# Kernel tuning notes

Measured on AMD Instinct MI355X. Metric: run time of the kernel, lower is better.

The kernel has to match this reference:

```python
import jax, jax.numpy as jnp
import numpy as np

B, T, D = 32, 1024, 1024
H = 512        # LSTM units per direction
L = 3          # num_layers


def _run_lstm(x, mask, W, U, b):
    """Masked unidirectional LSTM, Keras gate order (i, f, c, o).
    x: [B,T,D], mask: [B,T] bool (True = valid). Masked steps carry state
    and repeat the previous output, matching Keras masking semantics."""
    z_all = jnp.einsum('btd,dk->tbk', x, W) + b          # [T,B,4H]
    m_all = jnp.transpose(mask, (1, 0))                   # [T,B]

    def step(carry, inp):
        h, c = carry
        z_t, m_t = inp
        z = z_t + h @ U                                   # [B,4H]
        i, f, g, o = jnp.split(z, 4, axis=-1)
        i = jax.nn.sigmoid(i)
        f = jax.nn.sigmoid(f)
        g = jnp.tanh(g)
        o = jax.nn.sigmoid(o)
        c_new = f * c + i * g
        h_new = o * jnp.tanh(c_new)
        m = m_t[:, None]
        h = jnp.where(m, h_new, h)
        c = jnp.where(m, c_new, c)
        return (h, c), h

    h0 = jnp.zeros((x.shape[0], U.shape[0]), x.dtype)
    (_, _), hs = jax.lax.scan(step, (h0, h0), (z_all, m_all))
    return jnp.transpose(hs, (1, 0, 2))                   # [B,T,H]


def _bilstm(x, mask, Wf, Uf, bf, Wb, Ub, bb):
    fwd = _run_lstm(x, mask, Wf, Uf, bf)
    bwd = _run_lstm(x[:, ::-1], mask[:, ::-1], Wb, Ub, bb)[:, ::-1]
    return jnp.concatenate([fwd, bwd], axis=-1)           # [B,T,2H]


def setup_inputs() -> dict:
    key = jax.random.key(0)
    ks = jax.random.split(key, 16)
    s = 0.05
    inp = {
        'x': jax.random.normal(ks[0], (B, T, D), jnp.float32),
        'x_mask': jax.random.randint(ks[1], (B, T), 0, 2, jnp.int32),
        # stacked BiLSTM params (all layers share shapes since 2H == D)
        'Wf': jax.random.normal(ks[2], (L, D, 4 * H), jnp.float32) * s,
        'Uf': jax.random.normal(ks[3], (L, H, 4 * H), jnp.float32) * s,
        'bf': jax.random.normal(ks[4], (L, 4 * H), jnp.float32) * s,
        'Wb': jax.random.normal(ks[5], (L, D, 4 * H), jnp.float32) * s,
        'Ub': jax.random.normal(ks[6], (L, H, 4 * H), jnp.float32) * s,
        'bb': jax.random.normal(ks[7], (L, 4 * H), jnp.float32) * s,
        # task heads
        'Wp': jax.random.normal(ks[8], (2 * H, 2), jnp.float32) * s,
        'bp': jnp.zeros((2,), jnp.float32),
        'Wbu': jax.random.normal(ks[9], (2 * H, 2), jnp.float32) * s,
        'bbu': jnp.zeros((2,), jnp.float32),
        'Wss3': jax.random.normal(ks[10], (2 * H, 3), jnp.float32) * s,
        'bss3': jnp.zeros((3,), jnp.float32),
        'Wss8': jax.random.normal(ks[11], (2 * H, 8), jnp.float32) * s,
        'bss8': jnp.zeros((8,), jnp.float32),
        'training': 0,
    }
    return inp


def reference(x, x_mask, Wf, Uf, bf, Wb, Ub, bb, Wp, bp, Wbu, bbu,
              Wss3, bss3, Wss8, bss8, training):
    # mask = not(x_mask == 1): True = valid position
    mask = x_mask != 1
    for l in range(L):
        x = _bilstm(x, mask, Wf[l], Uf[l], bf[l], Wb[l], Ub[l], bb[l])
    x = jax.nn.relu(x)
    # dropout is identity at inference (training == 0)
    ppi = jax.nn.softmax(x @ Wp + bp, axis=-1)
    buried = x @ Wbu + bbu
    ss3 = x @ Wss3 + bss3
    ss8 = x @ Wss8 + bss8
    return (ppi, buried, ss3, ss8)
```

## Files before the change

### kernel.cpp

```cpp
#include <hip/hip_runtime.h>
#include <hip/hip_bf16.h>
#include <math.h>


#define B_ 32
#define T_ 1024
#define H_ 512
#define NG 2048

typedef __attribute__((ext_vector_type(8))) short bf16x8;
typedef __attribute__((ext_vector_type(4))) float f32x4;
typedef unsigned int u32;
typedef unsigned long long u64;
typedef unsigned short u16;

__device__ inline u16 f2bf(float f) {
    u32 u = __float_as_uint(f);
    return (u16)((u + 0x7fffu + ((u >> 16) & 1u)) >> 16);
}
__device__ inline float bf2f(u16 v) { return __uint_as_float(((u32)v) << 16); }
__device__ inline void gload16(const void* g, void* l) {
    __builtin_amdgcn_global_load_lds(
        (const __attribute__((address_space(1))) u32*)g,
        (__attribute__((address_space(3))) u32*)l, 16, 0, 0);
}
__device__ inline float fsig(float x) { return 1.0f / (1.0f + __expf(-x)); }
__device__ inline float ftanh(float x) { return 1.0f - 2.0f / (__expf(2.0f * x) + 1.0f); }

__global__ void zero_mem(float* __restrict__ s, int n) {
    int i = blockIdx.x * 256 + threadIdx.x;
    if (i < n) s[i] = 0.0f;
}

__global__ __launch_bounds__(256) void conv_bf16(const float* __restrict__ src,
                                                 u16* __restrict__ dst) {
    int i = blockIdx.x * 256 + threadIdx.x;
    float4 v = *(const float4*)&src[(size_t)i * 4];
    ushort4 o = { f2bf(v.x), f2bf(v.y), f2bf(v.z), f2bf(v.w) };
    *(ushort4*)&dst[(size_t)i * 4] = o;
}

__global__ __launch_bounds__(256) void transpose_w(const float* __restrict__ Wf,
                                                   const float* __restrict__ Wb,
                                                   u16* __restrict__ wt) {
    int mat = blockIdx.z;
    const float* W = ((mat & 1) ? Wb : Wf) + (size_t)(mat >> 1) * 1024 * NG;
    u16* dst = wt + (size_t)mat * NG * 1024;
    __shared__ float tile[64][65];
    int n0 = blockIdx.x * 64, k0 = blockIdx.y * 64;
    int t = threadIdx.x;
#pragma unroll
    for (int i = 0; i < 16; ++i) {
        int idx = t + i * 256;
        int kk = idx >> 6, nn = idx & 63;
        tile[kk][nn] = W[(size_t)(k0 + kk) * NG + n0 + nn];
    }
    __syncthreads();
#pragma unroll
    for (int i = 0; i < 16; ++i) {
        int idx = t + i * 256;
        int nn = idx >> 6, kk = idx & 63;
        dst[(size_t)(n0 + nn) * 1024 + k0 + kk] = f2bf(tile[kk][nn]);
    }
}

__global__ __launch_bounds__(256) void pack_u(const float* __restrict__ Uf,
                                              const float* __restrict__ Ub,
                                              u16* __restrict__ upk) {
    int mat = blockIdx.y;
    const float* U = ((mat & 1) ? Ub : Uf) + (size_t)(mat >> 1) * H_ * NG;
    u16* dst = upk + (size_t)mat * 1048576;
    int f = blockIdx.x * 256 + threadIdx.x;
    int lane = f & 63, ks = (f >> 6) & 15, c2 = (f >> 10) & 1;
    int cp = (f >> 11) & 3, wg = f >> 13;
    int col = cp * H_ + wg * 32 + c2 * 16 + (lane & 15);
    int krow = ks * 32 + (lane >> 4) * 8;
    u16 o[8];
#pragma unroll
    for (int j = 0; j < 8; ++j) o[j] = f2bf(U[(size_t)(krow + j) * NG + col]);
    *(uint4*)(dst + (size_t)f * 8) = *(uint4*)o;
}

__global__ __launch_bounds__(512, 1) void fused_layer(
    const u16* __restrict__ act,
    const u16* __restrict__ wtf, const u16* __restrict__ wtb,
    const float* __restrict__ bfl, const float* __restrict__ bbl,
    u16* __restrict__ zf, u16* __restrict__ zb,
    const u16* __restrict__ upk,
    const int* __restrict__ xmask,
    u32* __restrict__ hbuf32,
    float* __restrict__ cst, float* __restrict__ hst,
    u32* __restrict__ flags,
    u32* __restrict__ cnt,
    u16* __restrict__ hseq) {
    const int bx = blockIdx.x;
    const int tid = threadIdx.x;
    const int wave = tid >> 6, lane = tid & 63;
    const int fr = lane & 15, fq = lane >> 4;

    __shared__ __align__(16) u16 sh[16384];
    __shared__ float sacc[32 * 132];

    if (bx >= 32) {
        const int g = bx - 32;
        const int dir = (g >= 64) ? 1 : 0;
        const int local = dir ? g - 64 : g;
        const u16* Bt = dir ? wtb : wtf;
        const float* bias = dir ? bbl : bfl;
        u16* Zb = dir ? zb : zf;
        u32* mycnt = cnt + dir * 8;
        u16* sA = sh;
        u16* sB = sh + 4096;
        const int r = tid >> 2, kp = (tid & 3) * 8;
        const int wr = (wave & 1) * 64, wc = (wave >> 1) * 32;
        for (int i = local; i < 4096; i += 64) {
            int tb_ord = i >> 9, within = i & 511;
            int b = within >> 4, nt = within & 15;
            int tb = dir ? 7 - tb_ord : tb_ord;
            int m0 = b * 1024 + tb * 128;
            int n0 = nt * 128;
            const size_t arow = (size_t)(m0 + r) * 1024;
            const size_t brow = (size_t)(n0 + r) * 1024;
            f32x4 acc[4][2] = {};
            for (int kc = 0; kc < 1024; kc += 32) {
                gload16(act + arow + kc + kp, sA + tid * 8);
                gload16(Bt + brow + kc + kp, sB + tid * 8);
                __syncthreads();
                bf16x8 af[4], bfr[2];
                const int fk = fq * 8;
#pragma unroll
                for (int ii = 0; ii < 4; ++ii)
                    af[ii] = *(const bf16x8*)&sA[(wr + ii * 16 + fr) * 32 + fk];
#pragma unroll
                for (int j = 0; j < 2; ++j)
                    bfr[j] = *(const bf16x8*)&sB[(wc + j * 16 + fr) * 32 + fk];
#pragma unroll
                for (int ii = 0; ii < 4; ++ii)
#pragma unroll
                    for (int j = 0; j < 2; ++j)
                        acc[ii][j] = __builtin_amdgcn_mfma_f32_16x16x32_bf16(
                            af[ii], bfr[j], acc[ii][j], 0, 0, 0);
                __syncthreads();
            }
            float bv[2]; int un[2], gn[2];
#pragma unroll
            for (int j = 0; j < 2; ++j) {
                int n = n0 + wc + j * 16 + fr;
                bv[j] = bias[n];
                un[j] = n & 511; gn[j] = n >> 9;
            }
#pragma unroll
            for (int ii = 0; ii < 4; ++ii) {
                int mb = m0 + wr + ii * 16 + fq * 4;
#pragma unroll
                for (int j = 0; j < 2; ++j)
#pragma unroll
                    for (int rr = 0; rr < 4; ++rr)
                        Zb[(size_t)(mb + rr) * 2048 + un[j] * 4 + gn[j]] =
                            f2bf(acc[ii][j][rr] + bv[j]);
            }
            __syncthreads();
            if (tid == 0) {
                __threadfence();
                __hip_atomic_fetch_add(mycnt + tb, 1u, __ATOMIC_RELAXED,
                                       __HIP_MEMORY_SCOPE_AGENT);
            }
        }
        return;
    }

    const int dir = bx >> 4, wgs = bx & 15, u0 = wgs * 32;
    const u64* z64 = (const u64*)(dir ? zb : zf);
    const u16* up = upk + dir * 1048576;
    u32* hb32 = hbuf32 + dir * 16384;
    u32* myflag = flags + dir * 16 + wgs;
    const u32* fbase = flags + dir * 16;
    const u32* ctb = cnt + dir * 8;
    const int cp = wave & 3, bt = wave >> 2;
    const int row = bt * 16 + fr;
    const int swz = (row & 7) << 4;

    bf16x8 uf0[16], uf1[16];
#pragma unroll
    for (int ks = 0; ks < 16; ++ks) {
        size_t base0 = (((size_t)(wgs * 4 + cp) * 2) * 16 + ks) * 512 + lane * 8;
        uf0[ks] = *(const bf16x8*)(up + base0);
        uf1[ks] = *(const bf16x8*)(up + base0 + 16 * 512);
    }

    const int b0p = tid >> 5, ul = tid & 31, b1p = b0p + 16, ug = u0 + ul;
    const int sidx = (dir * 16 + wgs) * 1024 + tid * 2;
    float c0r = cst[sidx], c1r = cst[sidx + 1];
    float h0r = hst[sidx], h1r = hst[sidx + 1];
    const size_t hs0 = (size_t)b0p * T_ * 1024 + dir * 512 + ug;
    const size_t hs1 = (size_t)b1p * T_ * 1024 + dir * 512 + ug;

    int haveb = -1;
    auto wait_tb = [&](int tb) {
        if (tb == haveb) return;
        const u32* cpp = ctb + tb;
        u32 v = 512;
        if (lane == 0) v = __hip_atomic_load(cpp, __ATOMIC_RELAXED,
                                             __HIP_MEMORY_SCOPE_AGENT);
        while (!__all(v >= 512)) {
            if (lane == 0) v = __hip_atomic_load(cpp, __ATOMIC_RELAXED,
                                                 __HIP_MEMORY_SCOPE_AGENT);
        }
        haveb = tb;
    };

    {
        u32 tmp[16];
#pragma unroll
        for (int k = 0; k < 16; ++k)
            tmp[k] = __hip_atomic_load(hb32 + k * 512 + tid, __ATOMIC_RELAXED,
                                       __HIP_MEMORY_SCOPE_AGENT);
#pragma unroll
        for (int k = 0; k < 16; ++k) {
            int idx = k * 512 + tid;
            int sb = (idx * 4) ^ (((idx >> 8) & 7) << 4);
            *(u32*)((char*)sh + sb) = tmp[k];
        }
    }
    u64 za0, za1; int mc0, mc1;
    {
        int tc = dir ? (T_ - 1) : 0;
        wait_tb(tc >> 7);
        za0 = __hip_atomic_load(z64 + (size_t)(b0p * T_ + tc) * 512 + ug,
                                __ATOMIC_RELAXED, __HIP_MEMORY_SCOPE_AGENT);
        za1 = __hip_atomic_load(z64 + (size_t)(b1p * T_ + tc) * 512 + ug,
                                __ATOMIC_RELAXED, __HIP_MEMORY_SCOPE_AGENT);
        mc0 = xmask[b0p * T_ + tc]; mc1 = xmask[b1p * T_ + tc];
    }
    __syncthreads();

    u16 hb0s = 0, hb1s = 0;
    for (int st = 0; st < T_; ++st) {
        const int t = dir ? (T_ - 1 - st) : st;
        u32* nx32 = hb32 + (((st & 1) ^ 1) ? 8192 : 0);

        f32x4 acc0 = {0, 0, 0, 0}, acc1 = {0, 0, 0, 0};
#pragma unroll
        for (int ks = 0; ks < 16; ++ks) {
            int abyte = (row * 1024 + ks * 64 + fq * 16) ^ swz;
            bf16x8 a = *(const bf16x8*)((const char*)sh + abyte);
            acc0 = __builtin_amdgcn_mfma_f32_16x16x32_bf16(a, uf0[ks], acc0, 0, 0, 0);
            acc1 = __builtin_amdgcn_mfma_f32_16x16x32_bf16(a, uf1[ks], acc1, 0, 0, 0);
        }
#pragma unroll
        for (int j = 0; j < 4; ++j) {
            int b = bt * 16 + fq * 4 + j;
            sacc[b * 132 + cp * 32 + fr] = acc0[j];
            sacc[b * 132 + cp * 32 + 16 + fr] = acc1[j];
        }
        __syncthreads();
        {
            const float* s0 = sacc + b0p * 132;
            const float* s1 = sacc + b1p * 132;
            float i0 = fsig(bf2f((u16)za0) + s0[ul]);
            float f0 = fsig(bf2f((u16)(za0 >> 16)) + s0[32 + ul]);
            float g0 = ftanh(bf2f((u16)(za0 >> 32)) + s0[64 + ul]);
            float o0 = fsig(bf2f((u16)(za0 >> 48)) + s0[96 + ul]);
            if (mc0 != 1) { c0r = f0 * c0r + i0 * g0; h0r = o0 * ftanh(c0r); }
            float i1 = fsig(bf2f((u16)za1) + s1[ul]);
            float f1 = fsig(bf2f((u16)(za1 >> 16)) + s1[32 + ul]);
            float g1 = ftanh(bf2f((u16)(za1 >> 32)) + s1[64 + ul]);
            float o1 = fsig(bf2f((u16)(za1 >> 48)) + s1[96 + ul]);
            if (mc1 != 1) { c1r = f1 * c1r + i1 * g1; h1r = o1 * ftanh(c1r); }
            hb0s = f2bf(h0r); hb1s = f2bf(h1r);
            u32 nb0 = __shfl_xor((u32)hb0s, 1, 64);
            u32 nb1 = __shfl_xor((u32)hb1s, 1, 64);
            if ((ul & 1) == 0) {
                u32 pk0 = (u32)hb0s | (nb0 << 16);
                u32 pk1 = (u32)hb1s | (nb1 << 16);
                __hip_atomic_store(nx32 + b0p * 256 + (ug >> 1), pk0,
                                   __ATOMIC_RELAXED, __HIP_MEMORY_SCOPE_AGENT);
                __hip_atomic_store(nx32 + b1p * 256 + (ug >> 1), pk1,
                                   __ATOMIC_RELAXED, __HIP_MEMORY_SCOPE_AGENT);
            }
        }
        __syncthreads();
        const u32 tgt = (u32)(st + 1);
        if (tid == 0)
            __hip_atomic_store(myflag, tgt, __ATOMIC_RELAXED,
                               __HIP_MEMORY_SCOPE_AGENT);
        hseq[hs0 + (size_t)t * 1024] = hb0s;
        hseq[hs1 + (size_t)t * 1024] = hb1s;
        u64 zn0 = 0, zn1 = 0; int mn0 = 0, mn1 = 0;
        {
            int stn = (st + 1 < T_) ? st + 1 : st;
            int tcn = dir ? (T_ - 1 - stn) : stn;
            wait_tb(tcn >> 7);
            zn0 = __hip_atomic_load(z64 + (size_t)(b0p * T_ + tcn) * 512 + ug,
                                    __ATOMIC_RELAXED, __HIP_MEMORY_SCOPE_AGENT);
            zn1 = __hip_atomic_load(z64 + (size_t)(b1p * T_ + tcn) * 512 + ug,
                                    __ATOMIC_RELAXED, __HIP_MEMORY_SCOPE_AGENT);
            mn0 = xmask[b0p * T_ + tcn]; mn1 = xmask[b1p * T_ + tcn];
        }
        {
            u32 v = 0xffffffffu;
            if (lane < 16)
                v = __hip_atomic_load(fbase + lane, __ATOMIC_RELAXED,
                                      __HIP_MEMORY_SCOPE_AGENT);
            while (!__all(v >= tgt)) {
                if (lane < 16)
                    v = __hip_atomic_load(fbase + lane, __ATOMIC_RELAXED,
                                          __HIP_MEMORY_SCOPE_AGENT);
            }
        }
        if (st + 1 < T_) {
            const u32* src = hb32 + (((st + 1) & 1) ? 8192 : 0);
            u32 tmp[16];
#pragma unroll
            for (int k = 0; k < 16; ++k)
                tmp[k] = __hip_atomic_load(src + k * 512 + tid, __ATOMIC_RELAXED,
                                           __HIP_MEMORY_SCOPE_AGENT);
#pragma unroll
            for (int k = 0; k < 16; ++k) {
                int idx = k * 512 + tid;
                int sb = (idx * 4) ^ (((idx >> 8) & 7) << 4);
                *(u32*)((char*)sh + sb) = tmp[k];
            }
        }
        za0 = zn0; za1 = zn1; mc0 = mn0; mc1 = mn1;
        __syncthreads();
    }
    cst[sidx] = c0r; cst[sidx + 1] = c1r;
    hst[sidx] = h0r; hst[sidx + 1] = h1r;
}

__global__ __launch_bounds__(256) void heads_kernel(
    const u16* __restrict__ xin,
    const float* __restrict__ Wp, const float* __restrict__ bp,
    const float* __restrict__ Wbu, const float* __restrict__ bbu,
    const float* __restrict__ Wss3, const float* __restrict__ bss3,
    const float* __restrict__ Wss8, const float* __restrict__ bss8,
    float* __restrict__ out) {
    const int r = blockIdx.x * 4 + (threadIdx.x >> 6);
    const int lane = threadIdx.x & 63;
    const u16* xr = xin + (size_t)r * 1024 + lane * 16;
    uint4 q0 = *(const uint4*)xr;
    uint4 q1 = *(const uint4*)(xr + 8);
    float xv[16];
    u32 qs[8] = { q0.x, q0.y, q0.z, q0.w, q1.x, q1.y, q1.z, q1.w };
#pragma unroll
    for (int i = 0; i < 8; ++i) {
        xv[i * 2]     = fmaxf(__uint_as_float((qs[i] & 0xffffu) << 16), 0.0f);
        xv[i * 2 + 1] = fmaxf(__uint_as_float(qs[i] & 0xffff0000u), 0.0f);
    }
    float acc[15] = {};
    const int k0 = lane * 16;
#pragma unroll
    for (int kk = 0; kk < 16; kk++) {
        float xk = xv[kk];
        int k = k0 + kk;
        acc[0] += xk * Wp[k * 2];      acc[1] += xk * Wp[k * 2 + 1];
        acc[2] += xk * Wbu[k * 2];     acc[3] += xk * Wbu[k * 2 + 1];
        acc[4] += xk * Wss3[k * 3];    acc[5] += xk * Wss3[k * 3 + 1];
        acc[6] += xk * Wss3[k * 3 + 2];
#pragma unroll
        for (int o = 0; o < 8; o++) acc[7 + o] += xk * Wss8[k * 8 + o];
    }
#pragma unroll
    for (int o = 0; o < 15; o++) {
#pragma unroll
        for (int off = 32; off; off >>= 1) acc[o] += __shfl_xor(acc[o], off, 64);
    }
    if (lane == 0) {
        float a0 = acc[0] + bp[0], a1 = acc[1] + bp[1];
        float mx = fmaxf(a0, a1);
        float e0 = expf(a0 - mx), e1 = expf(a1 - mx);
        float ssum = e0 + e1;
        out[(size_t)r * 2] = e0 / ssum;
        out[(size_t)r * 2 + 1] = e1 / ssum;
        float* ob = out + 65536;
        ob[r * 2] = acc[2] + bbu[0]; ob[r * 2 + 1] = acc[3] + bbu[1];
        float* o3 = out + 131072;
        o3[r * 3 + 0] = acc[4] + bss3[0];
        o3[r * 3 + 1] = acc[5] + bss3[1];
        o3[r * 3 + 2] = acc[6] + bss3[2];
        float* o8 = out + 229376;
#pragma unroll
        for (int o = 0; o < 8; o++) o8[r * 8 + o] = acc[7 + o] + bss8[o];
    }
}

extern "C" void kernel_launch(void* const* d_in, const int* in_sizes, int n_in,
                              void* d_out, int out_size, void* d_ws, size_t ws_size,
                              hipStream_t stream) {
    const float* x = (const float*)d_in[0];
    const int* xmask = (const int*)d_in[1];
    const float* Wf = (const float*)d_in[2];
    const float* Uf = (const float*)d_in[3];
    const float* bfp = (const float*)d_in[4];
    const float* Wb = (const float*)d_in[5];
    const float* Ub = (const float*)d_in[6];
    const float* bbp = (const float*)d_in[7];
    const float* Wp = (const float*)d_in[8];
    const float* bp = (const float*)d_in[9];
    const float* Wbu = (const float*)d_in[10];
    const float* bbu = (const float*)d_in[11];
    const float* Wss3 = (const float*)d_in[12];
    const float* bss3 = (const float*)d_in[13];
    const float* Wss8 = (const float*)d_in[14];
    const float* bss8 = (const float*)d_in[15];

    char* wsb = (char*)d_ws;
    u16* actA = (u16*)wsb;
    u16* actB = (u16*)(wsb + (64ull << 20));
    u16* wt   = (u16*)(wsb + (128ull << 20));
    u16* upk  = (u16*)(wsb + (152ull << 20));
    char* stb = wsb + (164ull << 20);
    u32* hbuf32 = (u32*)stb;
    float* cst = (float*)(stb + 131072);
    float* hst = (float*)(stb + 262144);
    u32* flags = (u32*)(stb + 393216);
    u32* cnt   = (u32*)(stb + 393344);
    const int stateFloats = (393344 + 64) / 4;

    size_t fixedB = 165ull << 20;
    u16* zf = (u16*)(wsb + fixedB);
    u16* zb = zf + (size_t)B_ * T_ * 2048;

    conv_bf16<<<dim3(8388608 / 256), 256, 0, stream>>>(x, actA);
    transpose_w<<<dim3(32, 16, 6), 256, 0, stream>>>(Wf, Wb, wt);
    pack_u<<<dim3(512, 6), 256, 0, stream>>>(Uf, Ub, upk);

    const u16* cur = actA;
    for (int l = 0; l < 3; l++) {
        u16* dst = (l & 1) ? actA : actB;
        zero_mem<<<dim3((stateFloats + 255) / 256), 256, 0, stream>>>(
            (float*)stb, stateFloats);
        u16* wtf = wt + (size_t)(l * 2 + 0) * NG * 1024;
        u16* wtb = wt + (size_t)(l * 2 + 1) * NG * 1024;
        const u16* upkl = upk + (size_t)l * 2 * 1048576;
        const float* bfl = bfp + l * NG;
        const float* bbl = bbp + l * NG;

        const u16* a_act = cur;
        const u16* a_wtf = wtf; const u16* a_wtb = wtb;
        const float* a_bf = bfl; const float* a_bb = bbl;
        u16* a_zf = zf; u16* a_zb = zb;
        const u16* a_up = upkl; const int* a_xm = xmask;
        u32* a_hb = hbuf32; float* a_cs = cst; float* a_hs = hst;
        u32* a_fl = flags; u32* a_cnt = cnt; u16* a_hseq = dst;
        void* kargs[] = { &a_act, &a_wtf, &a_wtb, &a_bf, &a_bb, &a_zf, &a_zb,
                          &a_up, &a_xm, &a_hb, &a_cs, &a_hs, &a_fl, &a_cnt,
                          &a_hseq };
        hipLaunchCooperativeKernel((void*)fused_layer, dim3(160), dim3(512),
                                   kargs, 0, stream);
        cur = dst;
    }
    heads_kernel<<<dim3(B_ * T_ / 4), 256, 0, stream>>>(
        cur, Wp, bp, Wbu, bbu, Wss3, bss3, Wss8, bss8, (float*)d_out);
}
```

Before: 11.72 ms.

## Assign recurrent workgroups by XCD so each direction shares one chiplet

```diff
diff --git a/kernel.cpp b/kernel.cpp
--- a/kernel.cpp
+++ b/kernel.cpp
@@ -7,6 +7,7 @@
 #define T_ 1024
 #define H_ 512
 #define NG 2048
+#define NWG 160
 
 typedef __attribute__((ext_vector_type(8))) short bf16x8;
 typedef __attribute__((ext_vector_type(4))) float f32x4;
@@ -92,19 +93,62 @@
     float* __restrict__ cst, float* __restrict__ hst,
     u32* __restrict__ flags,
     u32* __restrict__ cnt,
+    u32* __restrict__ claim,
     u16* __restrict__ hseq) {
-    const int bx = blockIdx.x;
     const int tid = threadIdx.x;
     const int wave = tid >> 6, lane = tid & 63;
     const int fr = lane & 15, fq = lane >> 4;
 
     __shared__ __align__(16) u16 sh[16384];
     __shared__ float sacc[32 * 132];
-
-    if (bx >= 32) {
-        const int g = bx - 32;
-        const int dir = (g >= 64) ? 1 : 0;
-        const int local = dir ? g - 64 : g;
+    __shared__ int s_role, s_dir, s_idx;
+
+    if (tid == 0) {
+        u32 myxcd = 0;
+        asm volatile("s_getreg_b32 %0, hwreg(HW_REG_XCC_ID)" : "=s"(myxcd));
+        myxcd &= 7;
+        int myslot = (int)__hip_atomic_fetch_add(&claim[myxcd], 1u,
+                         __ATOMIC_RELAXED, __HIP_MEMORY_SCOPE_AGENT);
+        int total;
+        do {
+            total = 0;
+#pragma unroll
+            for (int i = 0; i < 8; ++i)
+                total += (int)__hip_atomic_load(&claim[i], __ATOMIC_RELAXED,
+                                                __HIP_MEMORY_SCOPE_AGENT);
+        } while (total < NWG);
+        int cv[8];
+#pragma unroll
+        for (int i = 0; i < 8; ++i)
+            cv[i] = (int)__hip_atomic_load(&claim[i], __ATOMIC_RELAXED,
+                                           __HIP_MEMORY_SCOPE_AGENT);
+        int a = 0;
+        for (int i = 1; i < 8; ++i) if (cv[i] > cv[a]) a = i;
+        int b = -1, bc = -1;
+        for (int i = 0; i < 8; ++i)
+            if (i != a && cv[i] > bc) { bc = cv[i]; b = i; }
+        int role = 1, dir = 0, idx = 0;
+        if (cv[a] >= 16 && bc >= 16) {
+            if ((int)myxcd == a && myslot < 16) { role = 0; dir = 0; idx = myslot; }
+            else if ((int)myxcd == b && myslot < 16) { role = 0; dir = 1; idx = myslot; }
+        } else {
+            int g = (int)__hip_atomic_fetch_add(&claim[8], 1u,
+                         __ATOMIC_RELAXED, __HIP_MEMORY_SCOPE_AGENT);
+            if (g < 16) { role = 0; dir = 0; idx = g; }
+            else if (g < 32) { role = 0; dir = 1; idx = g - 16; }
+        }
+        if (role == 1)
+            idx = (int)__hip_atomic_fetch_add(&claim[9], 1u,
+                         __ATOMIC_RELAXED, __HIP_MEMORY_SCOPE_AGENT);
+        s_role = role; s_dir = dir; s_idx = idx;
+    }
+    __syncthreads();
+    const int role = s_role;
+
+    if (role == 1) {
+        const int p = s_idx;
+        const int dir = (p >= 64) ? 1 : 0;
+        const int local = p & 63;
         const u16* Bt = dir ? wtb : wtf;
         const float* bias = dir ? bbl : bfl;
         u16* Zb = dir ? zb : zf;
@@ -169,12 +213,12 @@
         return;
     }
 
-    const int dir = bx >> 4, wgs = bx & 15, u0 = wgs * 32;
+    const int dir = s_dir, wgs = s_idx, u0 = wgs * 32;
     const u64* z64 = (const u64*)(dir ? zb : zf);
     const u16* up = upk + dir * 1048576;
     u32* hb32 = hbuf32 + dir * 16384;
-    u32* myflag = flags + dir * 16 + wgs;
-    const u32* fbase = flags + dir * 16;
+    u32* myflag = flags + dir * 64 + wgs;
+    const u32* fbase = flags + dir * 64;
     const u32* ctb = cnt + dir * 8;
     const int cp = wave & 3, bt = wave >> 2;
     const int row = bt * 16 + fr;
@@ -415,8 +459,9 @@
     float* cst = (float*)(stb + 131072);
     float* hst = (float*)(stb + 262144);
     u32* flags = (u32*)(stb + 393216);
-    u32* cnt   = (u32*)(stb + 393344);
-    const int stateFloats = (393344 + 64) / 4;
+    u32* cnt   = (u32*)(stb + 393728);
+    u32* claim = (u32*)(stb + 393792);
+    const int stateFloats = (393792 + 64) / 4;
 
     size_t fixedB = 165ull << 20;
     u16* zf = (u16*)(wsb + fixedB);
@@ -443,11 +488,12 @@
         u16* a_zf = zf; u16* a_zb = zb;
         const u16* a_up = upkl; const int* a_xm = xmask;
         u32* a_hb = hbuf32; float* a_cs = cst; float* a_hs = hst;
-        u32* a_fl = flags; u32* a_cnt = cnt; u16* a_hseq = dst;
+        u32* a_fl = flags; u32* a_cnt = cnt; u32* a_cl = claim;
+        u16* a_hseq = dst;
         void* kargs[] = { &a_act, &a_wtf, &a_wtb, &a_bf, &a_bb, &a_zf, &a_zb,
                           &a_up, &a_xm, &a_hb, &a_cs, &a_hs, &a_fl, &a_cnt,
-                          &a_hseq };
-        hipLaunchCooperativeKernel((void*)fused_layer, dim3(160), dim3(512),
+                          &a_cl, &a_hseq };
+        hipLaunchCooperativeKernel((void*)fused_layer, dim3(NWG), dim3(512),
                                    kargs, 0, stream);
         cur = dst;
     }
```

Measured after the change: 9.990 ms, median of 2. 1.17x faster.
